# Kernel tuning notes

Hardware: AMD Instinct MI355X
Metric: run time of the kernel (lower is better)

## Reference

```python
import jax, jax.numpy as jnp
import numpy as np

B, S, T = 8, 32, 64
V = S * T        # 2048 flattened variables
P = 512          # prediction points
N = 2 * S        # neighbors per prediction point
I = 256          # input_dim
H, AD = 8, 32    # attn_heads, attn_dim
D = H * AD       # 256
M = 256          # mlp hidden dim
L = 2            # attn layers
R = 128          # resolution


def setup_inputs() -> dict:
    ks = iter(jax.random.split(jax.random.key(0), 64))
    def w(shape):
        return jax.random.normal(next(ks), shape, jnp.float32) / np.sqrt(shape[-2])
    inp = {
        "encoded": jax.random.normal(next(ks), (B, V, I), jnp.float32),
        "true_u": jax.random.uniform(next(ks), (B, V, 1), jnp.float32),
        "attn_mask": jnp.zeros((P, N), jnp.float32),
        "pred_points": jnp.sort(jax.random.randint(next(ks), (P,), 0, V)),
        "neighbor_index": jax.random.randint(next(ks), (P, N), 0, V),
    }
    for p in ("k", "v"):
        inp[p + "W1"] = w((L, H, I + 1, M)); inp[p + "b1"] = jnp.zeros((L, H, M))
        inp[p + "W2"] = w((L, H, M, M));     inp[p + "b2"] = jnp.zeros((L, H, M))
        inp[p + "W3"] = w((L, H, M, AD));    inp[p + "b3"] = jnp.zeros((L, H, AD))
    inp["ds_W"] = w((I, D)); inp["ds_b"] = jnp.zeros((D,))
    inp["ln1_g"] = jnp.ones((L, D)); inp["ln1_b"] = jnp.zeros((L, D))
    inp["ff_W1"] = w((L, D, D)); inp["ff_b1"] = jnp.zeros((L, D))
    inp["ff_W2"] = w((L, D, D)); inp["ff_b2"] = jnp.zeros((L, D))
    inp["ln2_g"] = jnp.ones((L, D)); inp["ln2_b"] = jnp.zeros((L, D))
    inp["de_W1"] = w((D, M)); inp["de_b1"] = jnp.zeros((M,))
    inp["de_W2"] = w((M, M)); inp["de_b2"] = jnp.zeros((M,))
    inp["de_W3"] = w((M, R)); inp["de_b3"] = jnp.zeros((R,))
    return inp


def _ln(x, g, b):
    mu = x.mean(-1, keepdims=True)
    var = ((x - mu) ** 2).mean(-1, keepdims=True)
    return (x - mu) * jax.lax.rsqrt(var + 1e-5) * g + b


def _kv(x, W1, b1, W2, b2, W3, b3):
    # x: [B,V,I+1]; W1: [L,H,I+1,M] -> per-layer per-head MLP, out [L,B,H,V,AD]
    h = jax.nn.relu(jnp.einsum('bvi,lhim->lbhvm', x, W1) + b1[:, None, :, None, :])
    h = jax.nn.relu(jnp.einsum('lbhvm,lhmn->lbhvn', h, W2) + b2[:, None, :, None, :])
    return jnp.einsum('lbhvm,lhmd->lbhvd', h, W3) + b3[:, None, :, None, :]


def _forward(encoded, true_u, attn_mask, kW1, kb1, kW2, kb2, kW3, kb3,
             vW1, vb1, vW2, vb2, vW3, vb3, ds_W, ds_b, ln1_g, ln1_b,
             ff_W1, ff_b1, ff_W2, ff_b2, ln2_g, ln2_b,
             de_W1, de_b1, de_W2, de_b2, de_W3, de_b3,
             pred_points, neighbor_index):
    attn_dim = kW3.shape[-1]
    n_heads = kW1.shape[1]
    merged = jnp.concatenate([encoded, true_u], axis=-1)        # [B,V,I+1]
    keys = _kv(merged, kW1, kb1, kW2, kb2, kW3, kb3)            # [L,B,H,V,d]
    vals = _kv(merged, vW1, vb1, vW2, vb2, vW3, vb3)            # [L,B,H,V,d]

    cur = encoded[:, pred_points, :]                            # [B,P,I]
    att_value = cur @ ds_W + ds_b                               # [B,P,D]
    nb, np_, dd = att_value.shape
    scale = attn_dim ** (-0.5)
    for l in range(keys.shape[0]):
        q = att_value.reshape(nb, np_, n_heads, attn_dim)       # [B,P,H,d]
        nk = keys[l][:, :, neighbor_index, :]                   # [B,H,P,N,d]
        nv = vals[l][:, :, neighbor_index, :]                   # [B,H,P,N,d]
        scores = (jnp.einsum('bphd,bhpnd->bphn', q, nk) - attn_mask[None, :, None, :]) * scale
        wts = jax.nn.softmax(scores, axis=-1)                   # [B,P,H,N]
        att = jnp.einsum('bphn,bhpnd->bphd', wts, nv).reshape(nb, np_, dd)
        att_value = _ln(att_value + att, ln1_g[l], ln1_b[l])
        ff = jax.nn.relu(att_value @ ff_W1[l] + ff_b1[l]) @ ff_W2[l] + ff_b2[l]
        att_value = _ln(att_value + ff, ln2_g[l], ln2_b[l])

    h = jax.nn.relu(att_value @ de_W1 + de_b1)
    h = jax.nn.relu(h @ de_W2 + de_b2)
    logits = h @ de_W3 + de_b3                                  # [B,P,R]
    res = logits.shape[-1]
    target = jnp.clip(jnp.floor(true_u * res).astype(jnp.int32), 0, res - 1)
    target = target[:, pred_points, :]                          # [B,P,1]
    logprob = jnp.log(jnp.float32(res)) + jax.nn.log_softmax(logits, axis=-1)
    picked = jnp.take_along_axis(logprob, target, axis=2)       # [B,P,1]
    return -picked.sum((1, 2))                                  # [B]


def reference(encoded, true_u, attn_mask, kW1, kb1, kW2, kb2, kW3, kb3,
              vW1, vb1, vW2, vb2, vW3, vb3, ds_W, ds_b, ln1_g, ln1_b,
              ff_W1, ff_b1, ff_W2, ff_b2, ln2_g, ln2_b,
              de_W1, de_b1, de_W2, de_b2, de_W3, de_b3,
              pred_points, neighbor_index):
    return _forward(encoded, true_u, attn_mask, kW1, kb1, kW2, kb2, kW3, kb3,
                    vW1, vb1, vW2, vb2, vW3, vb3, ds_W, ds_b, ln1_g, ln1_b,
                    ff_W1, ff_b1, ff_W2, ff_b2, ln2_g, ln2_b,
                    de_W1, de_b1, de_W2, de_b2, de_W3, de_b3,
                    pred_points, neighbor_index)
```

## Files before the change

kernel.cpp:

```cpp
#include <hip/hip_runtime.h>
#include <hip/hip_bf16.h>
#include <cstdint>
#include <cstddef>

constexpr int Bc = 8;
constexpr int Vc = 2048;
constexpr int Pc = 512;
constexpr int Hc = 8;
constexpr int Lc = 2;
constexpr int ROWS_KV = Bc * Vc;
constexpr int ROWS_AT = Bc * Pc;

typedef __attribute__((ext_vector_type(8))) short bf16x8;
typedef __attribute__((ext_vector_type(4))) float f32x4;

static __device__ __forceinline__ unsigned short f2bf(float v) {
    __hip_bfloat16 h = __float2bfloat16(v);
    return *(unsigned short*)&h;
}
static __device__ __forceinline__ float bflo(unsigned int u) {
    return __uint_as_float(u << 16);
}
static __device__ __forceinline__ float bfhi(unsigned int u) {
    return __uint_as_float(u & 0xffff0000u);
}

__global__ __launch_bounds__(256) void prep_all_kernel(
    const float* kW1, const float* vW1, const float* kW2, const float* vW2,
    const float* kW3, const float* vW3,
    const float* ds_W, const float* ff_W1, const float* ff_W2,
    const float* de_W1, const float* de_W2, const float* de_W3,
    const float* encoded,
    unsigned short* __restrict__ W1t, unsigned short* __restrict__ W2t,
    unsigned short* __restrict__ W3t, unsigned short* __restrict__ Wm,
    unsigned short* __restrict__ Xbf)
{
    const int z = blockIdx.z;
    if (z >= 104) {
        const int idx = (z - 104) * 64 + blockIdx.y * 8 + blockIdx.x;
        if (idx >= 4096) return;
        const int i = idx * 256 + threadIdx.x;
        float4 v = ((const float4*)encoded)[i];
        ushort4 o;
        o.x = f2bf(v.x); o.y = f2bf(v.y); o.z = f2bf(v.z); o.w = f2bf(v.w);
        ((ushort4*)Xbf)[i] = o;
        return;
    }
    const float* src;
    unsigned short* dst;
    int C;
    if (z < 32) {
        const int net = z;
        src = ((net >> 4) ? vW1 : kW1) + (size_t)(net & 15) * 257 * 256;
        dst = W1t + (size_t)net * 65536;
        C = 256;
    } else if (z < 64) {
        const int net = z - 32;
        src = ((net >> 4) ? vW2 : kW2) + (size_t)(net & 15) * 256 * 256;
        dst = W2t + (size_t)net * 65536;
        C = 256;
    } else if (z < 96) {
        const int net = z - 64;
        src = ((net >> 4) ? vW3 : kW3) + (size_t)(net & 15) * 256 * 32;
        dst = W3t + (size_t)net * 8192;
        C = 32;
    } else {
        const int id = z - 96;
        const float* srcs[8] = {ds_W, ff_W1, ff_W1 + (size_t)65536,
                                ff_W2, ff_W2 + (size_t)65536, de_W1, de_W2, de_W3};
        src = srcs[id];
        dst = Wm + (size_t)id * 65536;
        C = (id == 7) ? 128 : 256;
    }
    if (blockIdx.x * 32 >= C) return;
    __shared__ float t[32][33];
    const int c0 = blockIdx.x * 32, k0 = blockIdx.y * 32;
    const int tx = threadIdx.x & 31, ty = threadIdx.x >> 5;
    #pragma unroll
    for (int i = 0; i < 32; i += 8)
        t[ty + i][tx] = src[(size_t)(k0 + ty + i) * C + (c0 + tx)];
    __syncthreads();
    #pragma unroll
    for (int i = 0; i < 32; i += 8)
        dst[(size_t)(c0 + ty + i) * 256 + (k0 + tx)] = f2bf(t[tx][ty + i]);
}

static __device__ __forceinline__ int hsw_chunk(int row, int ks, int quad) {
    int c = ks * 4 + quad;
    int p = c ^ (row & 31);
    return row * 256 + p * 8;
}
static __device__ __forceinline__ int hsw_elem(int row, int col) {
    int p = (col >> 3) ^ (row & 31);
    return row * 256 + p * 8 + (col & 7);
}

__global__ __launch_bounds__(512, 2) void kv_mfma_kernel(
    const unsigned short* __restrict__ Xbf, const float* __restrict__ true_u,
    const unsigned short* __restrict__ W1t, const unsigned short* __restrict__ W2t,
    const unsigned short* __restrict__ W3t,
    const float* __restrict__ kW1, const float* __restrict__ vW1,
    const float* __restrict__ kb1, const float* __restrict__ kb2, const float* __restrict__ kb3,
    const float* __restrict__ vb1, const float* __restrict__ vb2, const float* __restrict__ vb3,
    unsigned short* __restrict__ keys, unsigned short* __restrict__ vals)
{
    __shared__ unsigned short hbuf[64 * 256];
    __shared__ unsigned short w3buf[32 * 256];
    __shared__ float tub[64];

    const int tid = threadIdx.x;
    const int w = tid >> 6, lane = tid & 63;
    const int ln = lane & 15, quad = lane >> 4;
    const int lh = blockIdx.y, isv = blockIdx.z;
    const int net = isv * 16 + lh;
    const float* W1f = (isv ? vW1 : kW1) + (size_t)lh * 257 * 256;
    const float* b1  = (isv ? vb1 : kb1) + lh * 256;
    const float* b2  = (isv ? vb2 : kb2) + lh * 256;
    const float* b3  = (isv ? vb3 : kb3) + lh * 32;
    const unsigned short* w1 = W1t + (size_t)net * 65536;
    const unsigned short* w2 = W2t + (size_t)net * 65536;
    const unsigned short* w3 = W3t + (size_t)net * 8192;
    unsigned short* outp = isv ? vals : keys;
    const int base = blockIdx.x * 1024;
    const int cb = w * 32;

    bf16x8 B1[16], B2[16];
    {
        const unsigned short* p1 = w1 + (size_t)(cb + ln) * 256 + quad * 8;
        const unsigned short* p2 = w2 + (size_t)(cb + ln) * 256 + quad * 8;
        #pragma unroll
        for (int ks = 0; ks < 8; ++ks)
            #pragma unroll
            for (int ct = 0; ct < 2; ++ct) {
                B1[ks * 2 + ct] = *(const bf16x8*)(p1 + (size_t)ct * 16 * 256 + ks * 32);
                B2[ks * 2 + ct] = *(const bf16x8*)(p2 + (size_t)ct * 16 * 256 + ks * 32);
            }
    }
    {
        #pragma unroll
        for (int j = 0; j < 2; ++j) {
            const int cidx = tid * 2 + j;
            const int col = cidx >> 5, c = cidx & 31;
            uint4 d = *(const uint4*)(w3 + cidx * 8);
            *(uint4*)&w3buf[col * 256 + (c ^ (col & 31)) * 8] = d;
        }
    }
    float w1f[2], b1v[2], b2v[2];
    #pragma unroll
    for (int ct = 0; ct < 2; ++ct) {
        const int col = cb + ct * 16 + ln;
        w1f[ct] = W1f[256 * 256 + col];
        b1v[ct] = b1[col];
        b2v[ct] = b2[col];
    }
    const int rt3 = w & 3, ct3 = w >> 2;
    const float b3v = b3[ct3 * 16 + ln];

    const int b_ = base >> 11;
    const int l_ = lh >> 3, h_ = lh & 7;
    unsigned short* ob = outp + (((size_t)l_ * Bc + b_) * Vc) * 256 + h_ * 32;

    const f32x4 zero = {0.f, 0.f, 0.f, 0.f};
    const int xr = tid >> 3, cg = tid & 7;

    for (int t = 0; t < 16; ++t) {
        const int row0 = base + t * 64;
        __syncthreads();

        {
            const unsigned short* gx = Xbf + (size_t)(row0 + xr) * 256;
            #pragma unroll
            for (int j = 0; j < 4; ++j) {
                const int c = j * 8 + cg;
                uint4 d = *(const uint4*)(gx + c * 8);
                *(uint4*)&hbuf[xr * 256 + (c ^ (xr & 31)) * 8] = d;
            }
            if (tid < 64) tub[tid] = true_u[row0 + tid];
        }
        __syncthreads();

        f32x4 acc[4][2];
        #pragma unroll
        for (int rt = 0; rt < 4; ++rt)
            #pragma unroll
            for (int ct = 0; ct < 2; ++ct) acc[rt][ct] = zero;
        #pragma unroll
        for (int ks = 0; ks < 8; ++ks) {
            bf16x8 A[4];
            #pragma unroll
            for (int rt = 0; rt < 4; ++rt)
                A[rt] = *(const bf16x8*)&hbuf[hsw_chunk(rt * 16 + ln, ks, quad)];
            #pragma unroll
            for (int rt = 0; rt < 4; ++rt)
                #pragma unroll
                for (int ct = 0; ct < 2; ++ct)
                    acc[rt][ct] = __builtin_amdgcn_mfma_f32_16x16x32_bf16(A[rt], B1[ks * 2 + ct], acc[rt][ct], 0, 0, 0);
        }
        __syncthreads();
        #pragma unroll
        for (int ct = 0; ct < 2; ++ct) {
            const int col = cb + ct * 16 + ln;
            #pragma unroll
            for (int rt = 0; rt < 4; ++rt)
                #pragma unroll
                for (int r = 0; r < 4; ++r) {
                    const int row = rt * 16 + quad * 4 + r;
                    float v = fmaxf(acc[rt][ct][r] + b1v[ct] + tub[row] * w1f[ct], 0.f);
                    hbuf[hsw_elem(row, col)] = f2bf(v);
                }
        }
        __syncthreads();

        #pragma unroll
        for (int rt = 0; rt < 4; ++rt)
            #pragma unroll
            for (int ct = 0; ct < 2; ++ct) acc[rt][ct] = zero;
        #pragma unroll
        for (int ks = 0; ks < 8; ++ks) {
            bf16x8 A[4];
            #pragma unroll
            for (int rt = 0; rt < 4; ++rt)
                A[rt] = *(const bf16x8*)&hbuf[hsw_chunk(rt * 16 + ln, ks, quad)];
            #pragma unroll
            for (int rt = 0; rt < 4; ++rt)
                #pragma unroll
                for (int ct = 0; ct < 2; ++ct)
                    acc[rt][ct] = __builtin_amdgcn_mfma_f32_16x16x32_bf16(A[rt], B2[ks * 2 + ct], acc[rt][ct], 0, 0, 0);
        }
        __syncthreads();
        #pragma unroll
        for (int ct = 0; ct < 2; ++ct) {
            const int col = cb + ct * 16 + ln;
            #pragma unroll
            for (int rt = 0; rt < 4; ++rt)
                #pragma unroll
                for (int r = 0; r < 4; ++r) {
                    const int row = rt * 16 + quad * 4 + r;
                    hbuf[hsw_elem(row, col)] = f2bf(fmaxf(acc[rt][ct][r] + b2v[ct], 0.f));
                }
        }
        __syncthreads();

        f32x4 acc3 = zero;
        #pragma unroll
        for (int ks = 0; ks < 8; ++ks) {
            bf16x8 A  = *(const bf16x8*)&hbuf[hsw_chunk(rt3 * 16 + ln, ks, quad)];
            bf16x8 Bv = *(const bf16x8*)&w3buf[hsw_chunk(ct3 * 16 + ln, ks, quad)];
            acc3 = __builtin_amdgcn_mfma_f32_16x16x32_bf16(A, Bv, acc3, 0, 0, 0);
        }
        #pragma unroll
        for (int r = 0; r < 4; ++r) {
            const int grow = row0 + rt3 * 16 + quad * 4 + r;
            ob[(size_t)(grow & 2047) * 256 + ct3 * 16 + ln] = f2bf(acc3[r] + b3v);
        }
    }
}

__global__ __launch_bounds__(512) void decoder_kernel(
    const unsigned short* __restrict__ Xbf, const float* __restrict__ true_u,
    const unsigned short* __restrict__ keys, const unsigned short* __restrict__ vals,
    const int* __restrict__ nbr, const float* __restrict__ mask,
    const int* __restrict__ pp, const unsigned short* __restrict__ Wm,
    const float* __restrict__ ds_b,
    const float* __restrict__ ln1_g, const float* __restrict__ ln1_b,
    const float* __restrict__ ff_b1, const float* __restrict__ ff_b2,
    const float* __restrict__ ln2_g, const float* __restrict__ ln2_b,
    const float* __restrict__ de_b1, const float* __restrict__ de_b2,
    const float* __restrict__ de_b3, float* __restrict__ outp)
{
    __shared__ float avF[16][264];
    __shared__ float attF[16][264];
    __shared__ unsigned short abuf[16 * 256];
    __shared__ unsigned short hbuf[16 * 256];
    __shared__ int   ni_s[16][64];
    __shared__ float wtsb[16][64];
    __shared__ float psum[16][8], psq[16][8];
    __shared__ float rowmax[16];
    __shared__ int   tcol[16];
    __shared__ int   pps[16];

    const int tid = threadIdx.x;
    const int w = tid >> 6, lane = tid & 63;
    const int ln = lane & 15, quad = lane >> 4;
    const int bid = blockIdx.x;
    const int b = bid & 7;
    const int r0 = b * 512 + (bid >> 3) * 16;
    const int cb = w * 32;

    const f32x4 zero = {0.f, 0.f, 0.f, 0.f};

    if (tid < 16) pps[tid] = pp[(r0 + tid) & 511];
    #pragma unroll
    for (int j = 0; j < 2; ++j) {
        const int idx = tid * 2 + j;
        const int row = idx >> 6, n = idx & 63;
        ni_s[row][n] = nbr[((r0 + row) & 511) * 64 + n];
    }
    __syncthreads();

    {
        const int row = tid >> 5, c = tid & 31;
        const size_t arow = (size_t)b * Vc + pps[row];
        uint4 d = *(const uint4*)(Xbf + arow * 256 + c * 8);
        *(uint4*)&abuf[row * 256 + ((c ^ row) * 8)] = d;
    }
    __syncthreads();

    {
        const unsigned short* Wt = Wm;
        f32x4 acc[2]; acc[0] = zero; acc[1] = zero;
        const unsigned short* wb = Wt + (size_t)(cb + ln) * 256 + quad * 8;
        #pragma unroll
        for (int ks = 0; ks < 8; ++ks) {
            bf16x8 A = *(const bf16x8*)&abuf[hsw_chunk(ln, ks, quad)];
            #pragma unroll
            for (int ct = 0; ct < 2; ++ct) {
                bf16x8 Bv = *(const bf16x8*)(wb + (size_t)ct * 16 * 256 + ks * 32);
                acc[ct] = __builtin_amdgcn_mfma_f32_16x16x32_bf16(A, Bv, acc[ct], 0, 0, 0);
            }
        }
        __syncthreads();
        #pragma unroll
        for (int ct = 0; ct < 2; ++ct) {
            const int col = cb + ct * 16 + ln;
            const float bb = ds_b[col];
            #pragma unroll
            for (int r = 0; r < 4; ++r) {
                const int row = quad * 4 + r;
                float v = acc[ct][r] + bb;
                avF[row][col] = v;
                abuf[hsw_elem(row, col)] = f2bf(v);
            }
        }
    }
    __syncthreads();

    for (int l = 0; l < Lc; ++l) {
        const unsigned short* kvb = keys + (((size_t)l * Bc + b) * Vc) * 256;
        const unsigned short* vvb = vals + (((size_t)l * Bc + b) * Vc) * 256;

        {
            const int row0a = w * 2, row1a = w * 2 + 1;
            const int p0 = (r0 + row0a) & 511, p1 = (r0 + row1a) & 511;
            const int n = lane;
            const int vi0 = ni_s[row0a][n], vi1 = ni_s[row1a][n];
            const float m0 = mask[p0 * 64 + n], m1 = mask[p1 * 64 + n];
            const int nb4 = n >> 2, cg8 = (n & 3) * 8;
            int vrow0[4], vrow1[4];
            #pragma unroll
            for (int pass = 0; pass < 4; ++pass) {
                const int nn = pass * 16 + nb4;
                vrow0[pass] = ni_s[row0a][nn];
                vrow1[pass] = ni_s[row1a][nn];
            }
            for (int h = 0; h < 8; ++h) {
                uint4 vu0[4], vu1[4];
                #pragma unroll
                for (int pass = 0; pass < 4; ++pass) {
                    vu0[pass] = *(const uint4*)(vvb + (size_t)vrow0[pass] * 256 + h * 32 + cg8);
                    vu1[pass] = *(const uint4*)(vvb + (size_t)vrow1[pass] * 256 + h * 32 + cg8);
                }
                float q0[32], q1[32];
                #pragma unroll
                for (int j = 0; j < 8; ++j) {
                    float4 t0 = *(const float4*)&avF[row0a][h * 32 + j * 4];
                    float4 t1 = *(const float4*)&avF[row1a][h * 32 + j * 4];
                    q0[j * 4 + 0] = t0.x; q0[j * 4 + 1] = t0.y;
                    q0[j * 4 + 2] = t0.z; q0[j * 4 + 3] = t0.w;
                    q1[j * 4 + 0] = t1.x; q1[j * 4 + 1] = t1.y;
                    q1[j * 4 + 2] = t1.z; q1[j * 4 + 3] = t1.w;
                }
                const unsigned short* kp0 = kvb + (size_t)vi0 * 256 + h * 32;
                const unsigned short* kp1 = kvb + (size_t)vi1 * 256 + h * 32;
                float s0 = 0.f, s1 = 0.f;
                #pragma unroll
                for (int j = 0; j < 4; ++j) {
                    uint4 u0 = *(const uint4*)(kp0 + j * 8);
                    uint4 u1 = *(const uint4*)(kp1 + j * 8);
                    s0 += q0[j * 8 + 0] * bflo(u0.x) + q0[j * 8 + 1] * bfhi(u0.x);
                    s1 += q1[j * 8 + 0] * bflo(u1.x) + q1[j * 8 + 1] * bfhi(u1.x);
                    s0 += q0[j * 8 + 2] * bflo(u0.y) + q0[j * 8 + 3] * bfhi(u0.y);
                    s1 += q1[j * 8 + 2] * bflo(u1.y) + q1[j * 8 + 3] * bfhi(u1.y);
                    s0 += q0[j * 8 + 4] * bflo(u0.z) + q0[j * 8 + 5] * bfhi(u0.z);
                    s1 += q1[j * 8 + 4] * bflo(u1.z) + q1[j * 8 + 5] * bfhi(u1.z);
                    s0 += q0[j * 8 + 6] * bflo(u0.w) + q0[j * 8 + 7] * bfhi(u0.w);
                    s1 += q1[j * 8 + 6] * bflo(u1.w) + q1[j * 8 + 7] * bfhi(u1.w);
                }
                s0 = (s0 - m0) * 0.17677669529663689f;
                s1 = (s1 - m1) * 0.17677669529663689f;
                float mx0 = s0, mx1 = s1;
                #pragma unroll
                for (int off = 32; off >= 1; off >>= 1) {
                    mx0 = fmaxf(mx0, __shfl_xor(mx0, off));
                    mx1 = fmaxf(mx1, __shfl_xor(mx1, off));
                }
                float e0 = expf(s0 - mx0), e1 = expf(s1 - mx1);
                float sum0 = e0, sum1 = e1;
                #pragma unroll
                for (int off = 32; off >= 1; off >>= 1) {
                    sum0 += __shfl_xor(sum0, off);
                    sum1 += __shfl_xor(sum1, off);
                }
                wtsb[row0a][n] = e0 / sum0;
                wtsb[row1a][n] = e1 / sum1;
                float a0[8], a1[8];
                #pragma unroll
                for (int j = 0; j < 8; ++j) { a0[j] = 0.f; a1[j] = 0.f; }
                #pragma unroll
                for (int pass = 0; pass < 4; ++pass) {
                    const int nn = pass * 16 + nb4;
                    const float w0 = wtsb[row0a][nn], w1 = wtsb[row1a][nn];
                    uint4 u0 = vu0[pass];
                    uint4 u1 = vu1[pass];
                    a0[0] += w0 * bflo(u0.x); a0[1] += w0 * bfhi(u0.x);
                    a1[0] += w1 * bflo(u1.x); a1[1] += w1 * bfhi(u1.x);
                    a0[2] += w0 * bflo(u0.y); a0[3] += w0 * bfhi(u0.y);
                    a1[2] += w1 * bflo(u1.y); a1[3] += w1 * bfhi(u1.y);
                    a0[4] += w0 * bflo(u0.z); a0[5] += w0 * bfhi(u0.z);
                    a1[4] += w1 * bflo(u1.z); a1[5] += w1 * bfhi(u1.z);
                    a0[6] += w0 * bflo(u0.w); a0[7] += w0 * bfhi(u0.w);
                    a1[6] += w1 * bflo(u1.w); a1[7] += w1 * bfhi(u1.w);
                }
                #pragma unroll
                for (int off = 4; off <= 32; off <<= 1)
                    #pragma unroll
                    for (int j = 0; j < 8; ++j) {
                        a0[j] += __shfl_xor(a0[j], off);
                        a1[j] += __shfl_xor(a1[j], off);
                    }
                if (nb4 == 0)
                    #pragma unroll
                    for (int j = 0; j < 8; ++j) {
                        attF[row0a][h * 32 + cg8 + j] = a0[j];
                        attF[row1a][h * 32 + cg8 + j] = a1[j];
                    }
            }
            #pragma unroll
            for (int rr = 0; rr < 2; ++rr) {
                const int row = w * 2 + rr;
                const int c0 = lane * 4;
                float x[4];
                float sl = 0.f, ql = 0.f;
                #pragma unroll
                for (int j = 0; j < 4; ++j) {
                    x[j] = avF[row][c0 + j] + attF[row][c0 + j];
                    sl += x[j]; ql += x[j] * x[j];
                }
                #pragma unroll
                for (int off = 32; off >= 1; off >>= 1) {
                    sl += __shfl_xor(sl, off);
                    ql += __shfl_xor(ql, off);
                }
                const float mu = sl * (1.0f / 256.0f);
                const float var = ql * (1.0f / 256.0f) - mu * mu;
                const float rstd = 1.0f / sqrtf(fmaxf(var, 0.f) + 1e-5f);
                #pragma unroll
                for (int j = 0; j < 4; ++j) {
                    const int col = c0 + j;
                    float o = (x[j] - mu) * rstd * ln1_g[l * 256 + col] + ln1_b[l * 256 + col];
                    avF[row][col] = o;
                    abuf[hsw_elem(row, col)] = f2bf(o);
                }
            }
        }
        __syncthreads();

        {
            const unsigned short* W1 = Wm + (size_t)(1 + l) * 65536;
            f32x4 acc[2]; acc[0] = zero; acc[1] = zero;
            const unsigned short* wb = W1 + (size_t)(cb + ln) * 256 + quad * 8;
            #pragma unroll
            for (int ks = 0; ks < 8; ++ks) {
                bf16x8 A = *(const bf16x8*)&abuf[hsw_chunk(ln, ks, quad)];
                #pragma unroll
                for (int ct = 0; ct < 2; ++ct) {
                    bf16x8 Bv = *(const bf16x8*)(wb + (size_t)ct * 16 * 256 + ks * 32);
                    acc[ct] = __builtin_amdgcn_mfma_f32_16x16x32_bf16(A, Bv, acc[ct], 0, 0, 0);
                }
            }
            #pragma unroll
            for (int ct = 0; ct < 2; ++ct) {
                const int col = cb + ct * 16 + ln;
                const float bb = ff_b1[l * 256 + col];
                #pragma unroll
                for (int r = 0; r < 4; ++r) {
                    const int row = quad * 4 + r;
                    hbuf[hsw_elem(row, col)] = f2bf(fmaxf(acc[ct][r] + bb, 0.f));
                }
            }
        }
        __syncthreads();

        {
            const unsigned short* W2 = Wm + (size_t)(3 + l) * 65536;
            f32x4 acc[2]; acc[0] = zero; acc[1] = zero;
            const unsigned short* wb = W2 + (size_t)(cb + ln) * 256 + quad * 8;
            #pragma unroll
            for (int ks = 0; ks < 8; ++ks) {
                bf16x8 A = *(const bf16x8*)&hbuf[hsw_chunk(ln, ks, quad)];
                #pragma unroll
                for (int ct = 0; ct < 2; ++ct) {
                    bf16x8 Bv = *(const bf16x8*)(wb + (size_t)ct * 16 * 256 + ks * 32);
                    acc[ct] = __builtin_amdgcn_mfma_f32_16x16x32_bf16(A, Bv, acc[ct], 0, 0, 0);
                }
            }
            float vv[2][4];
            #pragma unroll
            for (int ct = 0; ct < 2; ++ct) {
                const int col = cb + ct * 16 + ln;
                const float bb = ff_b2[l * 256 + col];
                #pragma unroll
                for (int r = 0; r < 4; ++r) {
                    const int row = quad * 4 + r;
                    vv[ct][r] = acc[ct][r] + bb + avF[row][col];
                }
            }
            #pragma unroll
            for (int r = 0; r < 4; ++r) {
                float sl = vv[0][r] + vv[1][r];
                float ql = vv[0][r] * vv[0][r] + vv[1][r] * vv[1][r];
                #pragma unroll
                for (int off = 8; off >= 1; off >>= 1) {
                    sl += __shfl_xor(sl, off);
                    ql += __shfl_xor(ql, off);
                }
                if (ln == 0) {
                    const int row = quad * 4 + r;
                    psum[row][w] = sl; psq[row][w] = ql;
                }
            }
            __syncthreads();
            #pragma unroll
            for (int r = 0; r < 4; ++r) {
                const int row = quad * 4 + r;
                float sl = 0.f, ql = 0.f;
                #pragma unroll
                for (int j = 0; j < 8; ++j) { sl += psum[row][j]; ql += psq[row][j]; }
                const float mu = sl * (1.0f / 256.0f);
                const float var = ql * (1.0f / 256.0f) - mu * mu;
                const float rstd = 1.0f / sqrtf(fmaxf(var, 0.f) + 1e-5f);
                #pragma unroll
                for (int ct = 0; ct < 2; ++ct) {
                    const int col = cb + ct * 16 + ln;
                    float o = (vv[ct][r] - mu) * rstd * ln2_g[l * 256 + col] + ln2_b[l * 256 + col];
                    avF[row][col] = o;
                    abuf[hsw_elem(row, col)] = f2bf(o);
                }
            }
        }
        __syncthreads();
    }

    {
        const unsigned short* W1 = Wm + (size_t)5 * 65536;
        f32x4 acc[2]; acc[0] = zero; acc[1] = zero;
        const unsigned short* wb = W1 + (size_t)(cb + ln) * 256 + quad * 8;
        #pragma unroll
        for (int ks = 0; ks < 8; ++ks) {
            bf16x8 A = *(const bf16x8*)&abuf[hsw_chunk(ln, ks, quad)];
            #pragma unroll
            for (int ct = 0; ct < 2; ++ct) {
                bf16x8 Bv = *(const bf16x8*)(wb + (size_t)ct * 16 * 256 + ks * 32);
                acc[ct] = __builtin_amdgcn_mfma_f32_16x16x32_bf16(A, Bv, acc[ct], 0, 0, 0);
            }
        }
        #pragma unroll
        for (int ct = 0; ct < 2; ++ct) {
            const int col = cb + ct * 16 + ln;
            const float bb = de_b1[col];
            #pragma unroll
            for (int r = 0; r < 4; ++r) {
                const int row = quad * 4 + r;
                hbuf[hsw_elem(row, col)] = f2bf(fmaxf(acc[ct][r] + bb, 0.f));
            }
        }
    }
    __syncthreads();

    {
        const unsigned short* W2 = Wm + (size_t)6 * 65536;
        f32x4 acc[2]; acc[0] = zero; acc[1] = zero;
        const unsigned short* wb = W2 + (size_t)(cb + ln) * 256 + quad * 8;
        #pragma unroll
        for (int ks = 0; ks < 8; ++ks) {
            bf16x8 A = *(const bf16x8*)&hbuf[hsw_chunk(ln, ks, quad)];
            #pragma unroll
            for (int ct = 0; ct < 2; ++ct) {
                bf16x8 Bv = *(const bf16x8*)(wb + (size_t)ct * 16 * 256 + ks * 32);
                acc[ct] = __builtin_amdgcn_mfma_f32_16x16x32_bf16(A, Bv, acc[ct], 0, 0, 0);
            }
        }
        __syncthreads();
        #pragma unroll
        for (int ct = 0; ct < 2; ++ct) {
            const int col = cb + ct * 16 + ln;
            const float bb = de_b2[col];
            #pragma unroll
            for (int r = 0; r < 4; ++r) {
                const int row = quad * 4 + r;
                hbuf[hsw_elem(row, col)] = f2bf(fmaxf(acc[ct][r] + bb, 0.f));
            }
        }
    }
    __syncthreads();

    {
        const unsigned short* W3 = Wm + (size_t)7 * 65536;
        const int cb3 = w * 16;
        f32x4 a3 = zero;
        const unsigned short* wb = W3 + (size_t)(cb3 + ln) * 256 + quad * 8;
        #pragma unroll
        for (int ks = 0; ks < 8; ++ks) {
            bf16x8 A = *(const bf16x8*)&hbuf[hsw_chunk(ln, ks, quad)];
            bf16x8 Bv = *(const bf16x8*)(wb + ks * 32);
            a3 = __builtin_amdgcn_mfma_f32_16x16x32_bf16(A, Bv, a3, 0, 0, 0);
        }
        float lg[4];
        const float bb = de_b3[cb3 + ln];
        #pragma unroll
        for (int r = 0; r < 4; ++r) lg[r] = a3[r] + bb;

        #pragma unroll
        for (int r = 0; r < 4; ++r) {
            float m = lg[r];
            #pragma unroll
            for (int off = 8; off >= 1; off >>= 1) m = fmaxf(m, __shfl_xor(m, off));
            if (ln == 0) psum[quad * 4 + r][w] = m;
        }
        __syncthreads();
        if (tid < 16) {
            float m = psum[tid][0];
            #pragma unroll
            for (int j = 1; j < 8; ++j) m = fmaxf(m, psum[tid][j]);
            rowmax[tid] = m;
            float tu = true_u[(size_t)b * Vc + pps[tid]];
            int t = (int)floorf(tu * 128.0f);
            tcol[tid] = t < 0 ? 0 : (t > 127 ? 127 : t);
        }
        __syncthreads();
        #pragma unroll
        for (int r = 0; r < 4; ++r) {
            const int row = quad * 4 + r;
            const float mx = rowmax[row];
            const int t = tcol[row];
            float e = expf(lg[r] - mx);
            float xt = ((cb3 + ln) == t) ? lg[r] : 0.f;
            #pragma unroll
            for (int off = 8; off >= 1; off >>= 1) {
                e += __shfl_xor(e, off);
                xt += __shfl_xor(xt, off);
            }
            if (ln == 0) { psum[row][w] = e; psq[row][w] = xt; }
        }
        __syncthreads();
        float contrib = 0.f;
        if (tid < 16) {
            float sum = 0.f, xt = 0.f;
            #pragma unroll
            for (int j = 0; j < 8; ++j) { sum += psum[tid][j]; xt += psq[tid][j]; }
            const float lp = logf(128.0f) + (xt - rowmax[tid]) - logf(sum);
            contrib = -lp;
        }
        if (w == 0) {
            #pragma unroll
            for (int off = 32; off >= 1; off >>= 1) contrib += __shfl_xor(contrib, off);
            if (lane == 0) atomicAdd(&outp[b], contrib);
        }
    }
}

extern "C" void kernel_launch(void* const* d_in, const int* in_sizes, int n_in,
                              void* d_out, int out_size, void* d_ws, size_t ws_size,
                              hipStream_t stream)
{
    (void)in_sizes; (void)n_in; (void)out_size; (void)ws_size;

    const float* encoded        = (const float*)d_in[0];
    const float* true_u         = (const float*)d_in[1];
    const float* attn_mask      = (const float*)d_in[2];
    const int*   pred_points    = (const int*)d_in[3];
    const int*   neighbor_index = (const int*)d_in[4];
    const float* kW1 = (const float*)d_in[5];
    const float* kb1 = (const float*)d_in[6];
    const float* kW2 = (const float*)d_in[7];
    const float* kb2 = (const float*)d_in[8];
    const float* kW3 = (const float*)d_in[9];
    const float* kb3 = (const float*)d_in[10];
    const float* vW1 = (const float*)d_in[11];
    const float* vb1 = (const float*)d_in[12];
    const float* vW2 = (const float*)d_in[13];
    const float* vb2 = (const float*)d_in[14];
    const float* vW3 = (const float*)d_in[15];
    const float* vb3 = (const float*)d_in[16];
    const float* ds_W  = (const float*)d_in[17];
    const float* ds_b  = (const float*)d_in[18];
    const float* ln1_g = (const float*)d_in[19];
    const float* ln1_b = (const float*)d_in[20];
    const float* ff_W1 = (const float*)d_in[21];
    const float* ff_b1 = (const float*)d_in[22];
    const float* ff_W2 = (const float*)d_in[23];
    const float* ff_b2 = (const float*)d_in[24];
    const float* ln2_g = (const float*)d_in[25];
    const float* ln2_b = (const float*)d_in[26];
    const float* de_W1 = (const float*)d_in[27];
    const float* de_b1 = (const float*)d_in[28];
    const float* de_W2 = (const float*)d_in[29];
    const float* de_b2 = (const float*)d_in[30];
    const float* de_W3 = (const float*)d_in[31];
    const float* de_b3 = (const float*)d_in[32];

    float* out = (float*)d_out;

    constexpr size_t KV_ELEMS = (size_t)Lc * Bc * Hc * Vc * 32;
    unsigned short* keys = (unsigned short*)d_ws;
    unsigned short* vals = keys + KV_ELEMS;
    unsigned short* Xbf  = vals + KV_ELEMS;
    unsigned short* W1t  = Xbf + (size_t)ROWS_KV * 256;
    unsigned short* W2t  = W1t + (size_t)32 * 65536;
    unsigned short* W3t  = W2t + (size_t)32 * 65536;
    unsigned short* Wm   = W3t + (size_t)32 * 8192;

    (void)hipMemsetAsync(out, 0, Bc * sizeof(float), stream);

    prep_all_kernel<<<dim3(8, 8, 168), 256, 0, stream>>>(
        kW1, vW1, kW2, vW2, kW3, vW3,
        ds_W, ff_W1, ff_W2, de_W1, de_W2, de_W3, encoded,
        W1t, W2t, W3t, Wm, Xbf);

    kv_mfma_kernel<<<dim3(16, 16, 2), 512, 0, stream>>>(
        Xbf, true_u, W1t, W2t, W3t, kW1, vW1,
        kb1, kb2, kb3, vb1, vb2, vb3, keys, vals);

    decoder_kernel<<<dim3(ROWS_AT / 16), 512, 0, stream>>>(
        Xbf, true_u, keys, vals, neighbor_index, attn_mask, pred_points, Wm,
        ds_b, ln1_g, ln1_b, ff_b1, ff_b2, ln2_g, ln2_b,
        de_b1, de_b2, de_b3, out);
}
```

Before: 456.2 us.

## Double-buffer KV MLP shared memory, prefetch next tile, and transpose MFMA outputs

The per-head KV MLP kernel now uses two shared buffers that ping-pong between input and hidden activations. It prefetches the next 64-row input tile into registers during layer 2 and stores it after the second barrier, which drops several barriers per iteration. MFMA operands are swapped so each lane holds four consecutive columns, allowing vectorized 64-bit bias loads and packed bf16 stores to LDS and global memory. Shared memory per block doubles, which may limit occupancy, and extra prefetch registers add pressure under the 512x2 launch bounds.

Result: faster. 445.9 us (-2.2%).

```diff
diff --git a/kernel.cpp b/kernel.cpp
--- a/kernel.cpp
+++ b/kernel.cpp
@@ -94,6 +94,10 @@
     int p = (col >> 3) ^ (row & 31);
     return row * 256 + p * 8 + (col & 7);
 }
+static __device__ __forceinline__ int hsw_b64(int row, int col0) {
+    int c = col0 >> 3;
+    return row * 256 + ((c ^ (row & 31)) * 8) + (col0 & 7);
+}
 
 __global__ __launch_bounds__(512, 2) void kv_mfma_kernel(
     const unsigned short* __restrict__ Xbf, const float* __restrict__ true_u,
@@ -104,9 +108,10 @@
     const float* __restrict__ vb1, const float* __restrict__ vb2, const float* __restrict__ vb3,
     unsigned short* __restrict__ keys, unsigned short* __restrict__ vals)
 {
-    __shared__ unsigned short hbuf[64 * 256];
+    __shared__ unsigned short buf0[64 * 256];
+    __shared__ unsigned short buf1[64 * 256];
     __shared__ unsigned short w3buf[32 * 256];
-    __shared__ float tub[64];
+    __shared__ float tub[2][64];
 
     const int tid = threadIdx.x;
     const int w = tid >> 6, lane = tid & 63;
@@ -145,16 +150,16 @@
             *(uint4*)&w3buf[col * 256 + (c ^ (col & 31)) * 8] = d;
         }
     }
-    float w1f[2], b1v[2], b2v[2];
+    float4 b1v4[2], b2v4[2], w1f4[2];
     #pragma unroll
     for (int ct = 0; ct < 2; ++ct) {
-        const int col = cb + ct * 16 + ln;
-        w1f[ct] = W1f[256 * 256 + col];
-        b1v[ct] = b1[col];
-        b2v[ct] = b2[col];
+        const int col = cb + ct * 16 + quad * 4;
+        b1v4[ct] = *(const float4*)(b1 + col);
+        b2v4[ct] = *(const float4*)(b2 + col);
+        w1f4[ct] = *(const float4*)(W1f + 256 * 256 + col);
     }
     const int rt3 = w & 3, ct3 = w >> 2;
-    const float b3v = b3[ct3 * 16 + ln];
+    const float4 b3v4 = *(const float4*)(b3 + ct3 * 16 + quad * 4);
 
     const int b_ = base >> 11;
     const int l_ = lh >> 3, h_ = lh & 7;
@@ -163,96 +168,138 @@
     const f32x4 zero = {0.f, 0.f, 0.f, 0.f};
     const int xr = tid >> 3, cg = tid & 7;
 
+    {
+        const unsigned short* gx = Xbf + (size_t)(base + xr) * 256;
+        #pragma unroll
+        for (int j = 0; j < 4; ++j) {
+            const int c = j * 8 + cg;
+            uint4 d = *(const uint4*)(gx + c * 8);
+            *(uint4*)&buf0[xr * 256 + ((c ^ (xr & 31)) * 8)] = d;
+        }
+        if (tid < 64) tub[0][tid] = true_u[base + tid];
+    }
+    __syncthreads();
+
+    unsigned short* bufX = buf0;
+    unsigned short* bufH = buf1;
+
     for (int t = 0; t < 16; ++t) {
         const int row0 = base + t * 64;
-        __syncthreads();
-
+
+        f32x4 acc[4][2];
+        #pragma unroll
+        for (int rt = 0; rt < 4; ++rt) { acc[rt][0] = zero; acc[rt][1] = zero; }
         {
-            const unsigned short* gx = Xbf + (size_t)(row0 + xr) * 256;
+            bf16x8 A[4], An[4];
+            #pragma unroll
+            for (int rt = 0; rt < 4; ++rt)
+                A[rt] = *(const bf16x8*)&bufX[hsw_chunk(rt * 16 + ln, 0, quad)];
+            #pragma unroll
+            for (int ks = 0; ks < 8; ++ks) {
+                if (ks < 7) {
+                    #pragma unroll
+                    for (int rt = 0; rt < 4; ++rt)
+                        An[rt] = *(const bf16x8*)&bufX[hsw_chunk(rt * 16 + ln, ks + 1, quad)];
+                }
+                #pragma unroll
+                for (int rt = 0; rt < 4; ++rt)
+                    #pragma unroll
+                    for (int ct = 0; ct < 2; ++ct)
+                        acc[rt][ct] = __builtin_amdgcn_mfma_f32_16x16x32_bf16(
+                            B1[ks * 2 + ct], A[rt], acc[rt][ct], 0, 0, 0);
+                if (ks < 7) {
+                    #pragma unroll
+                    for (int rt = 0; rt < 4; ++rt) A[rt] = An[rt];
+                }
+            }
+        }
+        #pragma unroll
+        for (int rt = 0; rt < 4; ++rt) {
+            const int row = rt * 16 + ln;
+            const float tu = tub[t & 1][row];
+            #pragma unroll
+            for (int ct = 0; ct < 2; ++ct) {
+                const int col0 = cb + ct * 16 + quad * 4;
+                ushort4 o;
+                o.x = f2bf(fmaxf(acc[rt][ct][0] + b1v4[ct].x + tu * w1f4[ct].x, 0.f));
+                o.y = f2bf(fmaxf(acc[rt][ct][1] + b1v4[ct].y + tu * w1f4[ct].y, 0.f));
+                o.z = f2bf(fmaxf(acc[rt][ct][2] + b1v4[ct].z + tu * w1f4[ct].z, 0.f));
+                o.w = f2bf(fmaxf(acc[rt][ct][3] + b1v4[ct].w + tu * w1f4[ct].w, 0.f));
+                *(ushort4*)&bufH[hsw_b64(row, col0)] = o;
+            }
+        }
+        __syncthreads();
+
+        uint4 xp[4];
+        float tun = 0.f;
+        const bool havex = (t < 15);
+        if (havex) {
+            const unsigned short* gx = Xbf + (size_t)(row0 + 64 + xr) * 256;
+            #pragma unroll
+            for (int j = 0; j < 4; ++j)
+                xp[j] = *(const uint4*)(gx + (j * 8 + cg) * 8);
+            if (tid < 64) tun = true_u[row0 + 64 + tid];
+        }
+
+        #pragma unroll
+        for (int rt = 0; rt < 4; ++rt) { acc[rt][0] = zero; acc[rt][1] = zero; }
+        #pragma unroll
+        for (int ks = 0; ks < 8; ++ks) {
+            bf16x8 A[4];
+            #pragma unroll
+            for (int rt = 0; rt < 4; ++rt)
+                A[rt] = *(const bf16x8*)&bufH[hsw_chunk(rt * 16 + ln, ks, quad)];
+            #pragma unroll
+            for (int rt = 0; rt < 4; ++rt)
+                #pragma unroll
+                for (int ct = 0; ct < 2; ++ct)
+                    acc[rt][ct] = __builtin_amdgcn_mfma_f32_16x16x32_bf16(
+                        B2[ks * 2 + ct], A[rt], acc[rt][ct], 0, 0, 0);
+        }
+        #pragma unroll
+        for (int rt = 0; rt < 4; ++rt) {
+            const int row = rt * 16 + ln;
+            #pragma unroll
+            for (int ct = 0; ct < 2; ++ct) {
+                const int col0 = cb + ct * 16 + quad * 4;
+                ushort4 o;
+                o.x = f2bf(fmaxf(acc[rt][ct][0] + b2v4[ct].x, 0.f));
+                o.y = f2bf(fmaxf(acc[rt][ct][1] + b2v4[ct].y, 0.f));
+                o.z = f2bf(fmaxf(acc[rt][ct][2] + b2v4[ct].z, 0.f));
+                o.w = f2bf(fmaxf(acc[rt][ct][3] + b2v4[ct].w, 0.f));
+                *(ushort4*)&bufX[hsw_b64(row, col0)] = o;
+            }
+        }
+        __syncthreads();
+
+        if (havex) {
             #pragma unroll
             for (int j = 0; j < 4; ++j) {
                 const int c = j * 8 + cg;
-                uint4 d = *(const uint4*)(gx + c * 8);
-                *(uint4*)&hbuf[xr * 256 + (c ^ (xr & 31)) * 8] = d;
-            }
-            if (tid < 64) tub[tid] = true_u[row0 + tid];
-        }
-        __syncthreads();
-
-        f32x4 acc[4][2];
-        #pragma unroll
-        for (int rt = 0; rt < 4; ++rt)
-            #pragma unroll
-            for (int ct = 0; ct < 2; ++ct) acc[rt][ct] = zero;
+                *(uint4*)&bufH[xr * 256 + ((c ^ (xr & 31)) * 8)] = xp[j];
+            }
+            if (tid < 64) tub[(t + 1) & 1][tid] = tun;
+        }
+
+        f32x4 acc3 = zero;
         #pragma unroll
         for (int ks = 0; ks < 8; ++ks) {
-            bf16x8 A[4];
-            #pragma unroll
-            for (int rt = 0; rt < 4; ++rt)
-                A[rt] = *(const bf16x8*)&hbuf[hsw_chunk(rt * 16 + ln, ks, quad)];
-            #pragma unroll
-            for (int rt = 0; rt < 4; ++rt)
-                #pragma unroll
-                for (int ct = 0; ct < 2; ++ct)
-                    acc[rt][ct] = __builtin_amdgcn_mfma_f32_16x16x32_bf16(A[rt], B1[ks * 2 + ct], acc[rt][ct], 0, 0, 0);
-        }
-        __syncthreads();
-        #pragma unroll
-        for (int ct = 0; ct < 2; ++ct) {
-            const int col = cb + ct * 16 + ln;
-            #pragma unroll
-            for (int rt = 0; rt < 4; ++rt)
-                #pragma unroll
-                for (int r = 0; r < 4; ++r) {
-                    const int row = rt * 16 + quad * 4 + r;
-                    float v = fmaxf(acc[rt][ct][r] + b1v[ct] + tub[row] * w1f[ct], 0.f);
-                    hbuf[hsw_elem(row, col)] = f2bf(v);
-                }
-        }
-        __syncthreads();
-
-        #pragma unroll
-        for (int rt = 0; rt < 4; ++rt)
-            #pragma unroll
-            for (int ct = 0; ct < 2; ++ct) acc[rt][ct] = zero;
-        #pragma unroll
-        for (int ks = 0; ks < 8; ++ks) {
-            bf16x8 A[4];
-            #pragma unroll
-            for (int rt = 0; rt < 4; ++rt)
-                A[rt] = *(const bf16x8*)&hbuf[hsw_chunk(rt * 16 + ln, ks, quad)];
-            #pragma unroll
-            for (int rt = 0; rt < 4; ++rt)
-                #pragma unroll
-                for (int ct = 0; ct < 2; ++ct)
-                    acc[rt][ct] = __builtin_amdgcn_mfma_f32_16x16x32_bf16(A[rt], B2[ks * 2 + ct], acc[rt][ct], 0, 0, 0);
-        }
-        __syncthreads();
-        #pragma unroll
-        for (int ct = 0; ct < 2; ++ct) {
-            const int col = cb + ct * 16 + ln;
-            #pragma unroll
-            for (int rt = 0; rt < 4; ++rt)
-                #pragma unroll
-                for (int r = 0; r < 4; ++r) {
-                    const int row = rt * 16 + quad * 4 + r;
-                    hbuf[hsw_elem(row, col)] = f2bf(fmaxf(acc[rt][ct][r] + b2v[ct], 0.f));
-                }
-        }
-        __syncthreads();
-
-        f32x4 acc3 = zero;
-        #pragma unroll
-        for (int ks = 0; ks < 8; ++ks) {
-            bf16x8 A  = *(const bf16x8*)&hbuf[hsw_chunk(rt3 * 16 + ln, ks, quad)];
-            bf16x8 Bv = *(const bf16x8*)&w3buf[hsw_chunk(ct3 * 16 + ln, ks, quad)];
-            acc3 = __builtin_amdgcn_mfma_f32_16x16x32_bf16(A, Bv, acc3, 0, 0, 0);
-        }
-        #pragma unroll
-        for (int r = 0; r < 4; ++r) {
-            const int grow = row0 + rt3 * 16 + quad * 4 + r;
-            ob[(size_t)(grow & 2047) * 256 + ct3 * 16 + ln] = f2bf(acc3[r] + b3v);
-        }
+            bf16x8 Aw = *(const bf16x8*)&w3buf[hsw_chunk(ct3 * 16 + ln, ks, quad)];
+            bf16x8 Ah = *(const bf16x8*)&bufX[hsw_chunk(rt3 * 16 + ln, ks, quad)];
+            acc3 = __builtin_amdgcn_mfma_f32_16x16x32_bf16(Aw, Ah, acc3, 0, 0, 0);
+        }
+        {
+            const int grow = row0 + rt3 * 16 + ln;
+            ushort4 o;
+            o.x = f2bf(acc3[0] + b3v4.x);
+            o.y = f2bf(acc3[1] + b3v4.y);
+            o.z = f2bf(acc3[2] + b3v4.z);
+            o.w = f2bf(acc3[3] + b3v4.w);
+            *(ushort4*)(ob + (size_t)(grow & 2047) * 256 + ct3 * 16 + quad * 4) = o;
+        }
+        __syncthreads();
+
+        unsigned short* tmp = bufX; bufX = bufH; bufH = tmp;
     }
 }
 
```

## Restructure KV MLP kernel with async X prefetch, separate LDS buffers, wider per-wave tiles

Applied to the files above, without the earlier changes.

The KV MLP kernel now runs 256 threads per block, each wave owning 64 output columns, and each block handles a full 2048-row batch. The next X tile is prefetched with global_load_lds into a dedicated buffer while layers 2 and 3 compute, and three separate LDS buffers remove several barriers per tile. MFMA operands are swapped so each lane holds four consecutive columns, which lets the epilogue pack results with v_cvt_pk_bf16 into 64-bit LDS and global stores. The price is doubled weight registers per wave, one block per CU, and half as many blocks in the grid, which may lower occupancy and latency hiding.

New measurement: 495.8 us. 1.09x slower.

```diff
diff --git a/kernel.cpp b/kernel.cpp
--- a/kernel.cpp
+++ b/kernel.cpp
@@ -23,6 +23,11 @@
 }
 static __device__ __forceinline__ float bfhi(unsigned int u) {
     return __uint_as_float(u & 0xffff0000u);
+}
+static __device__ __forceinline__ unsigned int cvt2(float lo, float hi) {
+    unsigned int r;
+    asm("v_cvt_pk_bf16_f32 %0, %1, %2" : "=v"(r) : "v"(lo), "v"(hi));
+    return r;
 }
 
 __global__ __launch_bounds__(256) void prep_all_kernel(
@@ -94,8 +99,12 @@
     int p = (col >> 3) ^ (row & 31);
     return row * 256 + p * 8 + (col & 7);
 }
-
-__global__ __launch_bounds__(512, 2) void kv_mfma_kernel(
+static __device__ __forceinline__ int hsw_b64(int row, int col0) {
+    int c = col0 >> 3;
+    return row * 256 + ((c ^ (row & 31)) * 8) + (col0 & 7);
+}
+
+__global__ __launch_bounds__(256, 1) void kv_mfma_kernel(
     const unsigned short* __restrict__ Xbf, const float* __restrict__ true_u,
     const unsigned short* __restrict__ W1t, const unsigned short* __restrict__ W2t,
     const unsigned short* __restrict__ W3t,
@@ -104,9 +113,12 @@
     const float* __restrict__ vb1, const float* __restrict__ vb2, const float* __restrict__ vb3,
     unsigned short* __restrict__ keys, unsigned short* __restrict__ vals)
 {
-    __shared__ unsigned short hbuf[64 * 256];
+    __shared__ unsigned short bufX[64 * 256];
+    __shared__ unsigned short bufB[64 * 256];
+    __shared__ unsigned short bufC[64 * 256];
     __shared__ unsigned short w3buf[32 * 256];
-    __shared__ float tub[64];
+    __shared__ float b1f[256], b2f[256], w1r[256];
+    __shared__ float tub[2][64];
 
     const int tid = threadIdx.x;
     const int w = tid >> 6, lane = tid & 63;
@@ -121,138 +133,179 @@
     const unsigned short* w2 = W2t + (size_t)net * 65536;
     const unsigned short* w3 = W3t + (size_t)net * 8192;
     unsigned short* outp = isv ? vals : keys;
-    const int base = blockIdx.x * 1024;
-    const int cb = w * 32;
-
-    bf16x8 B1[16], B2[16];
+    const int base = blockIdx.x * 2048;
+    const int cb = w * 64;
+    constexpr int NT = 32;
+
+    bf16x8 B1[32], B2[32];
     {
         const unsigned short* p1 = w1 + (size_t)(cb + ln) * 256 + quad * 8;
         const unsigned short* p2 = w2 + (size_t)(cb + ln) * 256 + quad * 8;
         #pragma unroll
         for (int ks = 0; ks < 8; ++ks)
             #pragma unroll
-            for (int ct = 0; ct < 2; ++ct) {
-                B1[ks * 2 + ct] = *(const bf16x8*)(p1 + (size_t)ct * 16 * 256 + ks * 32);
-                B2[ks * 2 + ct] = *(const bf16x8*)(p2 + (size_t)ct * 16 * 256 + ks * 32);
+            for (int ct = 0; ct < 4; ++ct) {
+                B1[ks * 4 + ct] = *(const bf16x8*)(p1 + (size_t)ct * 16 * 256 + ks * 32);
+                B2[ks * 4 + ct] = *(const bf16x8*)(p2 + (size_t)ct * 16 * 256 + ks * 32);
             }
     }
     {
         #pragma unroll
-        for (int j = 0; j < 2; ++j) {
-            const int cidx = tid * 2 + j;
+        for (int j = 0; j < 4; ++j) {
+            const int cidx = tid * 4 + j;
             const int col = cidx >> 5, c = cidx & 31;
             uint4 d = *(const uint4*)(w3 + cidx * 8);
             *(uint4*)&w3buf[col * 256 + (c ^ (col & 31)) * 8] = d;
         }
     }
-    float w1f[2], b1v[2], b2v[2];
+    b1f[tid] = b1[tid];
+    b2f[tid] = b2[tid];
+    w1r[tid] = W1f[65536 + tid];
+
+    float4 b3v4[2];
     #pragma unroll
-    for (int ct = 0; ct < 2; ++ct) {
-        const int col = cb + ct * 16 + ln;
-        w1f[ct] = W1f[256 * 256 + col];
-        b1v[ct] = b1[col];
-        b2v[ct] = b2[col];
-    }
-    const int rt3 = w & 3, ct3 = w >> 2;
-    const float b3v = b3[ct3 * 16 + ln];
-
-    const int b_ = base >> 11;
+    for (int ct3 = 0; ct3 < 2; ++ct3)
+        b3v4[ct3] = *(const float4*)(b3 + ct3 * 16 + quad * 4);
+
+    const int b_ = blockIdx.x;
     const int l_ = lh >> 3, h_ = lh & 7;
     unsigned short* ob = outp + (((size_t)l_ * Bc + b_) * Vc) * 256 + h_ * 32;
 
     const f32x4 zero = {0.f, 0.f, 0.f, 0.f};
-    const int xr = tid >> 3, cg = tid & 7;
-
-    for (int t = 0; t < 16; ++t) {
+
+    auto stage_x = [&](int rowbase) {
+        #pragma unroll
+        for (int j = 0; j < 8; ++j) {
+            const int slot = (w * 8 + j) * 2;
+            const int r = slot + (lane >> 5);
+            const int c = (lane & 31) ^ (r & 31);
+            const unsigned short* src = Xbf + (size_t)(rowbase + r) * 256 + c * 8;
+            __builtin_amdgcn_global_load_lds(
+                (const __attribute__((address_space(1))) void*)src,
+                (__attribute__((address_space(3))) void*)&bufX[slot * 256],
+                16, 0, 0);
+        }
+    };
+
+    stage_x(base);
+    if (w == 0) {
+        const float* ts = true_u + base + lane;
+        __builtin_amdgcn_global_load_lds(
+            (const __attribute__((address_space(1))) void*)ts,
+            (__attribute__((address_space(3))) void*)&tub[0][0],
+            4, 0, 0);
+    }
+    __syncthreads();
+
+    for (int t = 0; t < NT; ++t) {
         const int row0 = base + t * 64;
-        __syncthreads();
-
-        {
-            const unsigned short* gx = Xbf + (size_t)(row0 + xr) * 256;
-            #pragma unroll
-            for (int j = 0; j < 4; ++j) {
-                const int c = j * 8 + cg;
-                uint4 d = *(const uint4*)(gx + c * 8);
-                *(uint4*)&hbuf[xr * 256 + (c ^ (xr & 31)) * 8] = d;
-            }
-            if (tid < 64) tub[tid] = true_u[row0 + tid];
-        }
-        __syncthreads();
-
-        f32x4 acc[4][2];
+
+        f32x4 acc[4][4];
         #pragma unroll
         for (int rt = 0; rt < 4; ++rt)
             #pragma unroll
-            for (int ct = 0; ct < 2; ++ct) acc[rt][ct] = zero;
+            for (int ct = 0; ct < 4; ++ct) acc[rt][ct] = zero;
         #pragma unroll
         for (int ks = 0; ks < 8; ++ks) {
             bf16x8 A[4];
             #pragma unroll
             for (int rt = 0; rt < 4; ++rt)
-                A[rt] = *(const bf16x8*)&hbuf[hsw_chunk(rt * 16 + ln, ks, quad)];
+                A[rt] = *(const bf16x8*)&bufX[hsw_chunk(rt * 16 + ln, ks, quad)];
             #pragma unroll
             for (int rt = 0; rt < 4; ++rt)
                 #pragma unroll
-                for (int ct = 0; ct < 2; ++ct)
-                    acc[rt][ct] = __builtin_amdgcn_mfma_f32_16x16x32_bf16(A[rt], B1[ks * 2 + ct], acc[rt][ct], 0, 0, 0);
-        }
-        __syncthreads();
-        #pragma unroll
-        for (int ct = 0; ct < 2; ++ct) {
-            const int col = cb + ct * 16 + ln;
-            #pragma unroll
-            for (int rt = 0; rt < 4; ++rt)
-                #pragma unroll
-                for (int r = 0; r < 4; ++r) {
-                    const int row = rt * 16 + quad * 4 + r;
-                    float v = fmaxf(acc[rt][ct][r] + b1v[ct] + tub[row] * w1f[ct], 0.f);
-                    hbuf[hsw_elem(row, col)] = f2bf(v);
-                }
-        }
-        __syncthreads();
+                for (int ct = 0; ct < 4; ++ct)
+                    acc[rt][ct] = __builtin_amdgcn_mfma_f32_16x16x32_bf16(
+                        B1[ks * 4 + ct], A[rt], acc[rt][ct], 0, 0, 0);
+        }
+        #pragma unroll
+        for (int rt = 0; rt < 4; ++rt) {
+            const int row = rt * 16 + ln;
+            const float tu = tub[t & 1][row];
+            #pragma unroll
+            for (int ct = 0; ct < 4; ++ct) {
+                const int col0 = cb + ct * 16 + quad * 4;
+                const float4 bb = *(const float4*)&b1f[col0];
+                const float4 wr = *(const float4*)&w1r[col0];
+                const float v0 = fmaxf(acc[rt][ct][0] + bb.x + tu * wr.x, 0.f);
+                const float v1 = fmaxf(acc[rt][ct][1] + bb.y + tu * wr.y, 0.f);
+                const float v2 = fmaxf(acc[rt][ct][2] + bb.z + tu * wr.z, 0.f);
+                const float v3 = fmaxf(acc[rt][ct][3] + bb.w + tu * wr.w, 0.f);
+                uint2 o; o.x = cvt2(v0, v1); o.y = cvt2(v2, v3);
+                *(uint2*)&bufB[hsw_b64(row, col0)] = o;
+            }
+        }
+        __syncthreads();
+
+        if (t + 1 < NT) {
+            stage_x(row0 + 64);
+            if (w == 0) {
+                const float* ts = true_u + row0 + 64 + lane;
+                __builtin_amdgcn_global_load_lds(
+                    (const __attribute__((address_space(1))) void*)ts,
+                    (__attribute__((address_space(3))) void*)&tub[(t + 1) & 1][0],
+                    4, 0, 0);
+            }
+        }
 
         #pragma unroll
         for (int rt = 0; rt < 4; ++rt)
             #pragma unroll
-            for (int ct = 0; ct < 2; ++ct) acc[rt][ct] = zero;
+            for (int ct = 0; ct < 4; ++ct) acc[rt][ct] = zero;
         #pragma unroll
         for (int ks = 0; ks < 8; ++ks) {
             bf16x8 A[4];
             #pragma unroll
             for (int rt = 0; rt < 4; ++rt)
-                A[rt] = *(const bf16x8*)&hbuf[hsw_chunk(rt * 16 + ln, ks, quad)];
+                A[rt] = *(const bf16x8*)&bufB[hsw_chunk(rt * 16 + ln, ks, quad)];
             #pragma unroll
             for (int rt = 0; rt < 4; ++rt)
                 #pragma unroll
-                for (int ct = 0; ct < 2; ++ct)
-                    acc[rt][ct] = __builtin_amdgcn_mfma_f32_16x16x32_bf16(A[rt], B2[ks * 2 + ct], acc[rt][ct], 0, 0, 0);
-        }
-        __syncthreads();
-        #pragma unroll
-        for (int ct = 0; ct < 2; ++ct) {
-            const int col = cb + ct * 16 + ln;
-            #pragma unroll
-            for (int rt = 0; rt < 4; ++rt)
-                #pragma unroll
-                for (int r = 0; r < 4; ++r) {
-                    const int row = rt * 16 + quad * 4 + r;
-                    hbuf[hsw_elem(row, col)] = f2bf(fmaxf(acc[rt][ct][r] + b2v[ct], 0.f));
-                }
-        }
-        __syncthreads();
-
-        f32x4 acc3 = zero;
+                for (int ct = 0; ct < 4; ++ct)
+                    acc[rt][ct] = __builtin_amdgcn_mfma_f32_16x16x32_bf16(
+                        B2[ks * 4 + ct], A[rt], acc[rt][ct], 0, 0, 0);
+        }
+        #pragma unroll
+        for (int rt = 0; rt < 4; ++rt) {
+            const int row = rt * 16 + ln;
+            #pragma unroll
+            for (int ct = 0; ct < 4; ++ct) {
+                const int col0 = cb + ct * 16 + quad * 4;
+                const float4 bb = *(const float4*)&b2f[col0];
+                const float v0 = fmaxf(acc[rt][ct][0] + bb.x, 0.f);
+                const float v1 = fmaxf(acc[rt][ct][1] + bb.y, 0.f);
+                const float v2 = fmaxf(acc[rt][ct][2] + bb.z, 0.f);
+                const float v3 = fmaxf(acc[rt][ct][3] + bb.w, 0.f);
+                uint2 o; o.x = cvt2(v0, v1); o.y = cvt2(v2, v3);
+                *(uint2*)&bufC[hsw_b64(row, col0)] = o;
+            }
+        }
+        asm volatile("s_waitcnt vmcnt(0)" ::: "memory");
+        __syncthreads();
+
+        f32x4 acc3[2]; acc3[0] = zero; acc3[1] = zero;
         #pragma unroll
         for (int ks = 0; ks < 8; ++ks) {
-            bf16x8 A  = *(const bf16x8*)&hbuf[hsw_chunk(rt3 * 16 + ln, ks, quad)];
-            bf16x8 Bv = *(const bf16x8*)&w3buf[hsw_chunk(ct3 * 16 + ln, ks, quad)];
-            acc3 = __builtin_amdgcn_mfma_f32_16x16x32_bf16(A, Bv, acc3, 0, 0, 0);
-        }
-        #pragma unroll
-        for (int r = 0; r < 4; ++r) {
-            const int grow = row0 + rt3 * 16 + quad * 4 + r;
-            ob[(size_t)(grow & 2047) * 256 + ct3 * 16 + ln] = f2bf(acc3[r] + b3v);
-        }
+            bf16x8 Ah = *(const bf16x8*)&bufC[hsw_chunk(w * 16 + ln, ks, quad)];
+            #pragma unroll
+            for (int ct3 = 0; ct3 < 2; ++ct3) {
+                bf16x8 Aw = *(const bf16x8*)&w3buf[hsw_chunk(ct3 * 16 + ln, ks, quad)];
+                acc3[ct3] = __builtin_amdgcn_mfma_f32_16x16x32_bf16(Aw, Ah, acc3[ct3], 0, 0, 0);
+            }
+        }
+        {
+            const int grow = row0 + w * 16 + ln;
+            #pragma unroll
+            for (int ct3 = 0; ct3 < 2; ++ct3) {
+                const float v0 = acc3[ct3][0] + b3v4[ct3].x;
+                const float v1 = acc3[ct3][1] + b3v4[ct3].y;
+                const float v2 = acc3[ct3][2] + b3v4[ct3].z;
+                const float v3 = acc3[ct3][3] + b3v4[ct3].w;
+                uint2 o; o.x = cvt2(v0, v1); o.y = cvt2(v2, v3);
+                *(uint2*)(ob + (size_t)(grow & 2047) * 256 + ct3 * 16 + quad * 4) = o;
+            }
+        }
+        __syncthreads();
     }
 }
 
@@ -727,7 +780,7 @@
         ds_W, ff_W1, ff_W2, de_W1, de_W2, de_W3, encoded,
         W1t, W2t, W3t, Wm, Xbf);
 
-    kv_mfma_kernel<<<dim3(16, 16, 2), 512, 0, stream>>>(
+    kv_mfma_kernel<<<dim3(8, 16, 2), 256, 0, stream>>>(
         Xbf, true_u, W1t, W2t, W3t, kW1, vW1,
         kb1, kb2, kb3, vb1, vb2, vb3, keys, vals);
 
```
